# Performance work log

Hardware: AMD Instinct MI355X
Metric: run time of the kernel (lower is better)

## Reference

```python
import jax, jax.numpy as jnp
import numpy as np

B, S, E, D, L, H = 8, 1024, 512, 1024, 8, 16
HD = D // H                 # 64
ROT = max(HD // 2, 32)      # 32
FF = 4 * D
FUSED = 3 * D + 2 * FF      # q,k,v,ff,ff_gate
EPS = 1e-5


def layer_norm(x, w, b):
    mu = jnp.mean(x, axis=-1, keepdims=True)
    var = jnp.mean(jnp.square(x - mu), axis=-1, keepdims=True)
    return (x - mu) * jax.lax.rsqrt(var + EPS) * w + b


def gelu(x):  # fused_gelu from source (erf form, constant 1.41421)
    return x * 0.5 * (1.0 + jax.scipy.special.erf(x / 1.41421))


def silu(x):
    return x * jax.nn.sigmoid(x)


def rotate_half(x):
    x1, x2 = jnp.split(x, 2, axis=-1)
    return jnp.concatenate([-x2, x1], axis=-1)


def rope_tables(seq_len):
    inv = 1.0 / (10000.0 ** (jnp.arange(0, ROT, 2, dtype=jnp.float32) / ROT))
    freqs = jnp.arange(seq_len, dtype=jnp.float32)[:, None] * inv[None, :]
    emb = jnp.concatenate([freqs, freqs], axis=-1)  # [S, ROT]
    # source caches sin/cos in bfloat16 (precision=torch.bfloat16)
    sin = jnp.sin(emb).astype(jnp.bfloat16).astype(jnp.float32)[None, None]
    cos = jnp.cos(emb).astype(jnp.bfloat16).astype(jnp.float32)[None, None]
    return sin, cos  # [1,1,S,ROT]


def setup_inputs() -> dict:
    key = jax.random.key(0)
    ks = jax.random.split(key, 24)
    std = 0.02
    inp = {
        "noisy_embeds": jax.random.normal(ks[0], (B, S, E), jnp.float32),
        "cond_embeds": jax.random.normal(ks[1], (B, S, E), jnp.float32),
        "prev_embeds": jax.random.normal(ks[2], (B, S, E), jnp.float32),
        "infill_mask": jax.random.uniform(ks[3], (B, S, 1), jnp.float32),
        "attention_mask": jnp.zeros((B, 1, 1, S), jnp.float32),
        "times": jax.random.uniform(ks[4], (B,), jnp.float32),
        # time embedding params
        "fourier_w": jax.random.normal(ks[5], (D // 2, 1), jnp.float32),
        "t1_w": jax.random.normal(ks[6], (D, D), jnp.float32) * std,
        "t1_b": jnp.zeros((D,), jnp.float32),
        "t2_w": jax.random.normal(ks[7], (D, D), jnp.float32) * std,
        "t2_b": jnp.zeros((D,), jnp.float32),
        # input projection
        "in_w": jax.random.normal(ks[8], (D, 4 * E), jnp.float32) * std,
        "in_b": jnp.zeros((D,), jnp.float32),
        # per-layer (stacked) block params
        "ln_w": jnp.ones((L, D), jnp.float32),
        "ln_b": jnp.zeros((L, D), jnp.float32),
        "cond_w": jax.random.normal(ks[9], (L, 2 * D, D), jnp.float32) * std,
        "cond_b": jnp.zeros((L, 2 * D), jnp.float32),
        "proj_w": jax.random.normal(ks[10], (L, FUSED, D), jnp.float32) * std,
        "attn_w": jax.random.normal(ks[11], (L, D, D), jnp.float32) * std,
        "attn_b": jnp.zeros((L, D), jnp.float32),
        "ff_w": jax.random.normal(ks[12], (L, D, FF), jnp.float32) * std,
        "ff_b": jnp.zeros((L, D), jnp.float32),
        # output head
        "outln_w": jnp.ones((D,), jnp.float32),
        "outln_b": jnp.zeros((D,), jnp.float32),
        "out_w": jax.random.normal(ks[13], (E, D), jnp.float32) * std,
        "out_b": jnp.zeros((E,), jnp.float32),
        "fin_w": jnp.ones((E,), jnp.float32),
        "fin_b": jnp.zeros((E,), jnp.float32),
    }
    return inp


def _split_heads(x):  # [B,S,H*hd] -> [B,H,S,hd]
    return x.reshape(B, S, H, HD).transpose(0, 2, 1, 3)


def _forward(noisy_embeds, cond_embeds, prev_embeds, infill_mask, attention_mask,
             times, fourier_w, t1_w, t1_b, t2_w, t2_b, in_w, in_b,
             ln_w, ln_b, cond_w, cond_b, proj_w, attn_w, attn_b, ff_w, ff_b,
             outln_w, outln_b, out_w, out_b, fin_w, fin_b):
    # -- time embedding (Random Fourier + MLP) --
    f = 2.0 * np.pi * (times[:, None] @ fourier_w.T)          # [B, D/2]
    te = jnp.concatenate([jnp.cos(f), jnp.sin(f)], axis=-1)   # [B, D]
    te = gelu(te @ t1_w.T + t1_b) @ t2_w.T + t2_b             # [B, D]
    time_embeds = te[:, None, :]                              # [B, 1, D]

    # -- input projection: cat(noisy, cond, prev, mask broadcast) --
    mask_feat = infill_mask * jnp.ones_like(noisy_embeds)     # [B,S,E]
    x = jnp.concatenate([noisy_embeds, cond_embeds, prev_embeds, mask_feat], axis=-1)
    h = x @ in_w.T + in_b                                     # [B,S,D]

    sin, cos = rope_tables(S)
    sm_scale = HD ** (-0.5)

    for i in range(L):
        units = layer_norm(h, ln_w[i], ln_b[i])
        # FiLM conditioning
        sb = silu(time_embeds) @ cond_w[i].T + cond_b[i]      # [B,1,2D]
        scale, bias = jnp.split(sb, 2, axis=-1)
        units = (1.0 + scale) * units + bias
        # fused projection and split
        proj = units @ proj_w[i].T                            # [B,S,11D]
        q, k, v, ff, ff_gate = jnp.split(
            proj, np.cumsum([D, D, D, FF])[:4].tolist(), axis=-1)
        q, k, v = _split_heads(q), _split_heads(k), _split_heads(v)  # [B,H,S,hd]
        # rotary on first ROT dims
        q = jnp.concatenate(
            [q[..., :ROT] * cos + rotate_half(q[..., :ROT]) * sin, q[..., ROT:]], axis=-1)
        k = jnp.concatenate(
            [k[..., :ROT] * cos + rotate_half(k[..., :ROT]) * sin, k[..., ROT:]], axis=-1)
        # NOTE: source scales BOTH q and k by hd^-0.5 (effective hd^-1)
        score = jnp.einsum('bhsd,bhSd->bhsS', q * sm_scale, k * sm_scale)
        score = score + attention_mask
        w = jax.nn.softmax(score, axis=-1)
        attn = jnp.einsum('bhsS,bhSd->bhsd', w, v)
        merged = attn.transpose(0, 2, 1, 3).reshape(B, S, D)
        attn_out = merged @ attn_w[i].T + attn_b[i]
        ff_out = (ff * gelu(ff_gate)) @ ff_w[i].T + ff_b[i]
        h = h + attn_out + ff_out

    out = layer_norm(h, outln_w, outln_b) @ out_w.T + out_b   # [B,S,E]
    return layer_norm(out, fin_w, fin_b)


def reference(noisy_embeds, cond_embeds, prev_embeds, infill_mask, attention_mask,
              times, fourier_w, t1_w, t1_b, t2_w, t2_b, in_w, in_b,
              ln_w, ln_b, cond_w, cond_b, proj_w, attn_w, attn_b, ff_w, ff_b,
              outln_w, outln_b, out_w, out_b, fin_w, fin_b):
    return _forward(noisy_embeds, cond_embeds, prev_embeds, infill_mask, attention_mask,
                    times, fourier_w, t1_w, t1_b, t2_w, t2_b, in_w, in_b,
                    ln_w, ln_b, cond_w, cond_b, proj_w, attn_w, attn_b, ff_w, ff_b,
                    outln_w, outln_b, out_w, out_b, fin_w, fin_b)
```

## Files before the change

### kernel.cpp

```cpp
#include <hip/hip_runtime.h>
#include <hip/hip_bf16.h>
#include <cstddef>
#include <cstdint>

#define BB 8
#define SS 1024
#define EE 512
#define DD 1024
#define LL 8
#define HH 16
#define HD 64
#define ROT 32
#define FF 4096
#define FUSED 11264
#define NTOK 8192

using u16 = unsigned short;
typedef __attribute__((ext_vector_type(8))) __bf16 bf16x8;
typedef __attribute__((ext_vector_type(4))) float f32x4;
typedef __attribute__((ext_vector_type(4))) unsigned short u16x4;
typedef __attribute__((ext_vector_type(8))) unsigned short u16x8;

typedef const __attribute__((address_space(1))) void gas_t;
typedef __attribute__((address_space(3))) void las_t;

__device__ __forceinline__ void gld16(const void* g, void* l) {
  __builtin_amdgcn_global_load_lds((gas_t*)g, (las_t*)l, 16, 0, 0);
}

__device__ __forceinline__ float bf2f(u16 u) {
  union { unsigned int i; float f; } v; v.i = ((unsigned int)u) << 16; return v.f;
}
__device__ __forceinline__ u16 f2bf(float f) {
  union { float f; unsigned int i; } v; v.f = f;
  unsigned int u = v.i;
  unsigned int r = u + 0x7FFFu + ((u >> 16) & 1u);
  return (u16)(r >> 16);
}
__device__ __forceinline__ float gelu_f(float x) {
  return x * 0.5f * (1.0f + erff(x / 1.41421f));
}
__device__ __forceinline__ float silu_f(float x) {
  return x / (1.0f + __expf(-x));
}

template <int ACCUM, int OUTBF16>
__global__ __launch_bounds__(256, 2) void gemm_bt(
    const u16* __restrict__ A, const u16* __restrict__ W,
    const float* __restrict__ bias, void* __restrict__ Cp,
    int M, int N, int K) {
  __shared__ __align__(16) u16 As[128 * 64];
  __shared__ __align__(16) u16 Bs[128 * 64];
  const int tid = threadIdx.x;
  const int w = tid >> 6, lane = tid & 63;
  const int m0 = blockIdx.y * 128, n0 = blockIdx.x * 128;
  const int wm = w >> 1, wn = w & 1;

  f32x4 acc[4][4] = {};

  for (int k0 = 0; k0 < K; k0 += 64) {
#pragma unroll
    for (int i = 0; i < 4; i++) {
      const int c = w + i * 4;
      const int r = c * 8 + (lane >> 3);
      const int colb = ((lane & 7) << 4) ^ ((r & 7) << 4);
      const u16* ga = A + (size_t)(m0 + r) * K + k0 + (colb >> 1);
      gld16(ga, &As[c * 512]);
      const u16* gb = W + (size_t)(n0 + r) * K + k0 + (colb >> 1);
      gld16(gb, &Bs[c * 512]);
    }
    __syncthreads();
#pragma unroll
    for (int ks = 0; ks < 2; ks++) {
      bf16x8 av[4], bv[4];
#pragma unroll
      for (int m = 0; m < 4; m++) {
        const int row = wm * 64 + m * 16 + (lane & 15);
        const int cb = (ks * 64 + ((lane >> 4) << 4)) ^ ((row & 7) << 4);
        av[m] = *(const bf16x8*)((const char*)As + row * 128 + cb);
      }
#pragma unroll
      for (int n = 0; n < 4; n++) {
        const int row = wn * 64 + n * 16 + (lane & 15);
        const int cb = (ks * 64 + ((lane >> 4) << 4)) ^ ((row & 7) << 4);
        bv[n] = *(const bf16x8*)((const char*)Bs + row * 128 + cb);
      }
#pragma unroll
      for (int m = 0; m < 4; m++)
#pragma unroll
        for (int n = 0; n < 4; n++)
          acc[m][n] = __builtin_amdgcn_mfma_f32_16x16x32_bf16(av[m], bv[n], acc[m][n], 0, 0, 0);
    }
    __syncthreads();
  }

  const int colb0 = n0 + wn * 64 + (lane & 15);
  const int rowb0 = m0 + wm * 64 + ((lane >> 4) << 2);
#pragma unroll
  for (int n = 0; n < 4; n++) {
    const int col = colb0 + n * 16;
    const float bn = bias ? bias[col] : 0.0f;
#pragma unroll
    for (int m = 0; m < 4; m++) {
#pragma unroll
      for (int r = 0; r < 4; r++) {
        const size_t idx = (size_t)(rowb0 + m * 16 + r) * N + col;
        const float v = acc[m][n][r] + bn;
        if (ACCUM) {
          ((float*)Cp)[idx] += v;
        } else if (OUTBF16) {
          ((u16*)Cp)[idx] = f2bf(v);
        } else {
          ((float*)Cp)[idx] = v;
        }
      }
    }
  }
}

__global__ __launch_bounds__(256, 2) void attn_fwd(
    const u16* __restrict__ qr, const u16* __restrict__ kr,
    const u16* __restrict__ vt, const float* __restrict__ mask,
    u16* __restrict__ merged) {
  __shared__ __align__(16) u16 Ks[2][128 * 64];
  __shared__ __align__(16) u16 Vs[2][64 * 128];
  __shared__ __align__(16) u16 Ps[4][16 * 128];
  const int tid = threadIdx.x, w = tid >> 6, lane = tid & 63;
  const int g = blockIdx.x;
  const int j = g >> 3;
  const int bh = (g & 7) + ((j >> 4) << 3);
  const int qx = j & 15;
  const int b = bh >> 4;
  const int q0 = qx * 64 + w * 16;
  const u16* Qb = qr + (size_t)bh * SS * HD;
  const u16* Kb = kr + (size_t)bh * SS * HD;
  const u16* Vb = vt + (size_t)bh * HD * SS;
  const float* mb = mask + (size_t)b * SS;

  bf16x8 qf0, qf1;
  {
    const int qrow = q0 + (lane & 15);
    const u16* qp = Qb + (size_t)qrow * HD + ((lane >> 4) << 3);
    qf0 = *(const bf16x8*)qp;
    qf1 = *(const bf16x8*)(qp + 32);
  }

  float mrun[4], srun[4];
  f32x4 acc[4] = {};
#pragma unroll
  for (int r = 0; r < 4; r++) { mrun[r] = -1e30f; srun[r] = 0.0f; }

  u16* pw = &Ps[w][0];

  auto stage = [&](int buf, int kv0) {
#pragma unroll
    for (int i = 0; i < 4; i++) {
      const int c = w + i * 4;
      {
        const int r = c * 8 + (lane >> 3);
        const int colb = ((lane & 7) << 4) ^ ((r & 7) << 4);
        gld16(Kb + (size_t)(kv0 + r) * HD + (colb >> 1), &Ks[buf][c * 512]);
      }
      {
        const int d = c * 4 + (lane >> 4);
        const int colb = ((lane & 15) << 4) ^ ((d & 7) << 4);
        gld16(Vb + (size_t)d * SS + kv0 + (colb >> 1), &Vs[buf][c * 512]);
      }
    }
  };

  stage(0, 0);
  __syncthreads();

  for (int t = 0; t < 8; t++) {
    const int cur = t & 1;
    const int kv0 = t * 128;
    if (t < 7) stage(cur ^ 1, kv0 + 128);

    f32x4 p[8];
    __builtin_amdgcn_s_setprio(1);
#pragma unroll
    for (int blk = 0; blk < 8; blk++) {
      const int row = blk * 16 + (lane & 15);
      const int swz = (row & 7) << 4;
      const bf16x8 k0v = *(const bf16x8*)((const char*)Ks[cur] + row * 128 + ((((lane >> 4) << 4)) ^ swz));
      const bf16x8 k1v = *(const bf16x8*)((const char*)Ks[cur] + row * 128 + ((64 + ((lane >> 4) << 4)) ^ swz));
      f32x4 z = {};
      p[blk] = __builtin_amdgcn_mfma_f32_16x16x32_bf16(qf0, k0v, z, 0, 0, 0);
      p[blk] = __builtin_amdgcn_mfma_f32_16x16x32_bf16(qf1, k1v, p[blk], 0, 0, 0);
    }
    __builtin_amdgcn_s_setprio(0);

    float mv[8];
#pragma unroll
    for (int blk = 0; blk < 8; blk++) mv[blk] = mb[kv0 + blk * 16 + (lane & 15)];
#pragma unroll
    for (int blk = 0; blk < 8; blk++)
#pragma unroll
      for (int r = 0; r < 4; r++) p[blk][r] = p[blk][r] * (1.0f / 64.0f) + mv[blk];

    float fac[4];
#pragma unroll
    for (int r = 0; r < 4; r++) {
      float tm = p[0][r];
#pragma unroll
      for (int blk = 1; blk < 8; blk++) tm = fmaxf(tm, p[blk][r]);
      tm = fmaxf(tm, __shfl_xor(tm, 1));
      tm = fmaxf(tm, __shfl_xor(tm, 2));
      tm = fmaxf(tm, __shfl_xor(tm, 4));
      tm = fmaxf(tm, __shfl_xor(tm, 8));
      const float mn = fmaxf(mrun[r], tm);
      fac[r] = __expf(mrun[r] - mn);
      mrun[r] = mn;
      float rs = 0.0f;
#pragma unroll
      for (int blk = 0; blk < 8; blk++) {
        const float e = __expf(p[blk][r] - mn);
        p[blk][r] = e;
        rs += e;
      }
      rs += __shfl_xor(rs, 1);
      rs += __shfl_xor(rs, 2);
      rs += __shfl_xor(rs, 4);
      rs += __shfl_xor(rs, 8);
      srun[r] = srun[r] * fac[r] + rs;
    }
#pragma unroll
    for (int dblk = 0; dblk < 4; dblk++)
#pragma unroll
      for (int r = 0; r < 4; r++) acc[dblk][r] *= fac[r];

#pragma unroll
    for (int blk = 0; blk < 8; blk++)
#pragma unroll
      for (int r = 0; r < 4; r++) {
        const int q = ((lane >> 4) << 2) + r;
        pw[(q * 128 + blk * 16 + (lane & 15)) ^ ((q & 7) << 3)] = f2bf(p[blk][r]);
      }

    bf16x8 pa[4];
#pragma unroll
    for (int ks = 0; ks < 4; ks++) {
      const int q = lane & 15;
      pa[ks] = *(const bf16x8*)(pw + ((q * 128 + ks * 32 + ((lane >> 4) << 3)) ^ ((q & 7) << 3)));
    }

    __builtin_amdgcn_s_setprio(1);
#pragma unroll
    for (int dblk = 0; dblk < 4; dblk++) {
      const int drow = dblk * 16 + (lane & 15);
      const int swz = (drow & 7) << 4;
#pragma unroll
      for (int ks = 0; ks < 4; ks++) {
        const bf16x8 vv = *(const bf16x8*)((const char*)Vs[cur] + drow * 256 + ((ks * 64 + ((lane >> 4) << 4)) ^ swz));
        acc[dblk] = __builtin_amdgcn_mfma_f32_16x16x32_bf16(pa[ks], vv, acc[dblk], 0, 0, 0);
      }
    }
    __builtin_amdgcn_s_setprio(0);

    __syncthreads();
  }

#pragma unroll
  for (int dblk = 0; dblk < 4; dblk++)
#pragma unroll
    for (int r = 0; r < 4; r++) {
      const int sq = q0 + ((lane >> 4) << 2) + r;
      const int d = dblk * 16 + (lane & 15);
      merged[((size_t)b * SS + sq) * DD + (bh & 15) * HD + d] = f2bf(acc[dblk][r] / srun[r]);
    }
}

__global__ __launch_bounds__(256) void ln_mod(
    const float* __restrict__ x, const float* __restrict__ lw,
    const float* __restrict__ lb, const float* __restrict__ sb,
    u16* __restrict__ out) {
  const int row = blockIdx.x, tid = threadIdx.x;
  const float4 v = ((const float4*)(x + (size_t)row * DD))[tid];
  float vv[4] = {v.x, v.y, v.z, v.w};
  float s = vv[0] + vv[1] + vv[2] + vv[3];
  float q = vv[0] * vv[0] + vv[1] * vv[1] + vv[2] * vv[2] + vv[3] * vv[3];
  for (int off = 1; off < 64; off <<= 1) {
    s += __shfl_xor(s, off);
    q += __shfl_xor(q, off);
  }
  __shared__ float red[8];
  const int w = tid >> 6, lane = tid & 63;
  if (lane == 0) { red[w] = s; red[4 + w] = q; }
  __syncthreads();
  s = red[0] + red[1] + red[2] + red[3];
  q = red[4] + red[5] + red[6] + red[7];
  const float mu = s * (1.0f / DD);
  const float inv = rsqrtf(q * (1.0f / DD) - mu * mu + 1e-5f);
  const int b = row >> 10;
  u16x4 o;
#pragma unroll
  for (int j = 0; j < 4; j++) {
    const int d = tid * 4 + j;
    float g = (vv[j] - mu) * inv * lw[d] + lb[d];
    if (sb) g = (1.0f + sb[(size_t)b * 2048 + d]) * g + sb[(size_t)b * 2048 + DD + d];
    o[j] = f2bf(g);
  }
  *(u16x4*)(out + (size_t)row * DD + tid * 4) = o;
}

__global__ __launch_bounds__(128) void ln_fin(
    const float* __restrict__ x, const float* __restrict__ w_,
    const float* __restrict__ b_, float* __restrict__ out) {
  const int row = blockIdx.x, tid = threadIdx.x;
  const float4 v = ((const float4*)(x + (size_t)row * EE))[tid];
  float vv[4] = {v.x, v.y, v.z, v.w};
  float s = vv[0] + vv[1] + vv[2] + vv[3];
  float q = vv[0] * vv[0] + vv[1] * vv[1] + vv[2] * vv[2] + vv[3] * vv[3];
  for (int off = 1; off < 64; off <<= 1) {
    s += __shfl_xor(s, off);
    q += __shfl_xor(q, off);
  }
  __shared__ float red[4];
  const int w = tid >> 6, lane = tid & 63;
  if (lane == 0) { red[w] = s; red[2 + w] = q; }
  __syncthreads();
  s = red[0] + red[1];
  q = red[2] + red[3];
  const float mu = s * (1.0f / EE);
  const float inv = rsqrtf(q * (1.0f / EE) - mu * mu + 1e-5f);
  float4 o;
  o.x = (vv[0] - mu) * inv * w_[tid * 4 + 0] + b_[tid * 4 + 0];
  o.y = (vv[1] - mu) * inv * w_[tid * 4 + 1] + b_[tid * 4 + 1];
  o.z = (vv[2] - mu) * inv * w_[tid * 4 + 2] + b_[tid * 4 + 2];
  o.w = (vv[3] - mu) * inv * w_[tid * 4 + 3] + b_[tid * 4 + 3];
  ((float4*)(out + (size_t)row * EE))[tid] = o;
}

template <int IA, int OA>
__global__ __launch_bounds__(256) void vec_gemm(
    const float* __restrict__ in, const float* __restrict__ W,
    const float* __restrict__ bias, float* __restrict__ out, int N, int K) {
  const int n = blockIdx.x * 256 + threadIdx.x;
  const int b = blockIdx.y, l = blockIdx.z;
  const float* ir = in + (size_t)b * K;
  const float* wr = W + ((size_t)l * N + n) * K;
  float s = bias[(size_t)l * N + n];
  for (int k = 0; k < K; k += 4) {
    float4 a = *(const float4*)(ir + k);
    const float4 ww = *(const float4*)(wr + k);
    if (IA) { a.x = silu_f(a.x); a.y = silu_f(a.y); a.z = silu_f(a.z); a.w = silu_f(a.w); }
    s += a.x * ww.x + a.y * ww.y + a.z * ww.z + a.w * ww.w;
  }
  if (OA) s = gelu_f(s);
  out[((size_t)l * gridDim.y + b) * N + n] = s;
}

__global__ void time_fourier(const float* __restrict__ times,
                             const float* __restrict__ fw, float* __restrict__ te0) {
  const int j = blockIdx.x * 256 + threadIdx.x;
  const int b = blockIdx.y;
  const float f = 6.28318530717958647692f * times[b] * fw[j];
  te0[(size_t)b * DD + j] = cosf(f);
  te0[(size_t)b * DD + 512 + j] = sinf(f);
}

__global__ void rope_tab(float* __restrict__ st, float* __restrict__ ct) {
  const int s = blockIdx.x;
  const int j = threadIdx.x;
  const int i = j & 15;
  const float inv = powf(10000.0f, -(float)i * (1.0f / 16.0f));
  const float f = (float)s * inv;
  st[s * 32 + j] = bf2f(f2bf(sinf(f)));
  ct[s * 32 + j] = bf2f(f2bf(cosf(f)));
}

__global__ void build_x(const float* __restrict__ a, const float* __restrict__ b,
                        const float* __restrict__ c, const float* __restrict__ m,
                        u16* __restrict__ x) {
  const size_t i4 = ((size_t)blockIdx.x * 256 + threadIdx.x) * 4;
  if (i4 >= (size_t)NTOK * 2048) return;
  const size_t tok = i4 >> 11;
  const int e = (int)(i4 & 2047);
  float4 v;
  if (e < 512)       v = *(const float4*)(a + tok * 512 + e);
  else if (e < 1024) v = *(const float4*)(b + tok * 512 + (e - 512));
  else if (e < 1536) v = *(const float4*)(c + tok * 512 + (e - 1024));
  else { const float mm = m[tok]; v = make_float4(mm, mm, mm, mm); }
  u16x4 o;
  o[0] = f2bf(v.x); o[1] = f2bf(v.y); o[2] = f2bf(v.z); o[3] = f2bf(v.w);
  *(u16x4*)(x + i4) = o;
}

__global__ void rope_qk(const u16* __restrict__ proj, const float* __restrict__ st,
                        const float* __restrict__ ct, u16* __restrict__ q,
                        u16* __restrict__ k) {
  const size_t idx = (size_t)blockIdx.x * 256 + threadIdx.x;
  const size_t tok = idx >> 10;
  const int hd = (int)(idx & 1023);
  const int hh = hd >> 6, d = hd & 63;
  const int s = (int)(tok & 1023);
  const size_t bb = tok >> 10;
  const u16* pr = proj + tok * FUSED;
  float qv = bf2f(pr[hd]);
  float kv = bf2f(pr[DD + hd]);
  if (d < ROT) {
    const float cs = ct[s * 32 + d], sn = st[s * 32 + d];
    const int pidx = hd - d + ((d < 16) ? d + 16 : d - 16);
    const float qp = bf2f(pr[pidx]);
    const float kp = bf2f(pr[DD + pidx]);
    const float sg = (d < 16) ? -1.0f : 1.0f;
    qv = qv * cs + sg * qp * sn;
    kv = kv * cs + sg * kp * sn;
  }
  const size_t o = ((bb * HH + hh) * SS + s) * HD + d;
  q[o] = f2bf(qv);
  k[o] = f2bf(kv);
}

__global__ __launch_bounds__(256) void transp_v(const u16* __restrict__ proj,
                                                u16* __restrict__ v) {
  __shared__ u16 tile[64 * 72];
  const int tid = threadIdx.x;
  const int s0 = blockIdx.x * 64, h = blockIdx.y, b = blockIdx.z;
  {
    const int sl = tid >> 2, qd = (tid & 3) * 16;
    const u16* src = proj + (size_t)(b * SS + s0 + sl) * FUSED + 2 * DD + h * 64 + qd;
    const u16x8 a0 = *(const u16x8*)src;
    const u16x8 a1 = *(const u16x8*)(src + 8);
    *(u16x8*)&tile[sl * 72 + qd] = a0;
    *(u16x8*)&tile[sl * 72 + qd + 8] = a1;
  }
  __syncthreads();
  {
    const int dl = tid >> 2, qs = (tid & 3) * 16;
    u16x8 o0, o1;
#pragma unroll
    for (int j = 0; j < 8; j++) o0[j] = tile[(qs + j) * 72 + dl];
#pragma unroll
    for (int j = 0; j < 8; j++) o1[j] = tile[(qs + 8 + j) * 72 + dl];
    u16* dst = v + ((size_t)(b * HH + h) * HD + dl) * SS + s0 + qs;
    *(u16x8*)dst = o0;
    *(u16x8*)(dst + 8) = o1;
  }
}

__global__ void gate_k(const u16* __restrict__ proj, u16* __restrict__ ff) {
  const size_t i8 = ((size_t)blockIdx.x * 256 + threadIdx.x) * 8;
  const size_t tok = i8 >> 12;
  const int f = (int)(i8 & 4095);
  const u16* pr = proj + tok * FUSED + 3 * DD + f;
  const u16x8 a = *(const u16x8*)pr;
  const u16x8 g = *(const u16x8*)(pr + FF);
  u16x8 o;
#pragma unroll
  for (int j = 0; j < 8; j++) o[j] = f2bf(bf2f(a[j]) * gelu_f(bf2f(g[j])));
  *(u16x8*)(ff + i8) = o;
}

__global__ void cast_bf16(const float* __restrict__ in, u16* __restrict__ out, size_t n4) {
  const size_t i = (size_t)blockIdx.x * 256 + threadIdx.x;
  if (i >= n4) return;
  const float4 v = ((const float4*)in)[i];
  u16x4 o;
  o[0] = f2bf(v.x); o[1] = f2bf(v.y); o[2] = f2bf(v.z); o[3] = f2bf(v.w);
  ((u16x4*)out)[i] = o;
}

extern "C" void kernel_launch(void* const* d_in, const int* in_sizes, int n_in,
                              void* d_out, int out_size, void* d_ws, size_t ws_size,
                              hipStream_t stream) {
  const float* noisy   = (const float*)d_in[0];
  const float* condi   = (const float*)d_in[1];
  const float* prev    = (const float*)d_in[2];
  const float* infill  = (const float*)d_in[3];
  const float* amask   = (const float*)d_in[4];
  const float* times   = (const float*)d_in[5];
  const float* fourier = (const float*)d_in[6];
  const float* t1_w    = (const float*)d_in[7];
  const float* t1_b    = (const float*)d_in[8];
  const float* t2_w    = (const float*)d_in[9];
  const float* t2_b    = (const float*)d_in[10];
  const float* in_w    = (const float*)d_in[11];
  const float* in_b    = (const float*)d_in[12];
  const float* ln_w    = (const float*)d_in[13];
  const float* ln_b    = (const float*)d_in[14];
  const float* cond_w  = (const float*)d_in[15];
  const float* cond_b  = (const float*)d_in[16];
  const float* proj_w  = (const float*)d_in[17];
  const float* attn_w  = (const float*)d_in[18];
  const float* attn_b  = (const float*)d_in[19];
  const float* ff_w    = (const float*)d_in[20];
  const float* ff_b    = (const float*)d_in[21];
  const float* outln_w = (const float*)d_in[22];
  const float* outln_b = (const float*)d_in[23];
  const float* out_w   = (const float*)d_in[24];
  const float* out_b   = (const float*)d_in[25];
  const float* fin_w   = (const float*)d_in[26];
  const float* fin_b   = (const float*)d_in[27];
  float* outp = (float*)d_out;

  char* p = (char*)d_ws;
  auto alloc = [&](size_t bytes) -> char* {
    char* r = p;
    p += (bytes + 255) & ~(size_t)255;
    return r;
  };
  u16* in_w_h   = (u16*)alloc((size_t)DD * 2048 * 2);
  u16* proj_w_h = (u16*)alloc((size_t)LL * FUSED * DD * 2);
  u16* attn_w_h = (u16*)alloc((size_t)LL * DD * DD * 2);
  u16* ff_w_h   = (u16*)alloc((size_t)LL * DD * FF * 2);
  u16* out_w_h  = (u16*)alloc((size_t)EE * DD * 2);
  float* te0 = (float*)alloc((size_t)BB * DD * 4);
  float* te1 = (float*)alloc((size_t)BB * DD * 4);
  float* te2 = (float*)alloc((size_t)BB * DD * 4);
  float* sb  = (float*)alloc((size_t)LL * BB * 2048 * 4);
  float* stab = (float*)alloc((size_t)SS * 32 * 4);
  float* ctab = (float*)alloc((size_t)SS * 32 * 4);
  u16* xb    = (u16*)alloc((size_t)NTOK * 2048 * 2);
  float* h   = (float*)alloc((size_t)NTOK * DD * 4);
  u16* units = (u16*)alloc((size_t)NTOK * DD * 2);
  u16* projb = (u16*)alloc((size_t)NTOK * FUSED * 2);
  u16* qrb   = (u16*)alloc((size_t)NTOK * DD * 2);
  u16* krb   = (u16*)alloc((size_t)NTOK * DD * 2);
  u16* vtb   = (u16*)alloc((size_t)NTOK * DD * 2);
  u16* mg    = (u16*)alloc((size_t)NTOK * DD * 2);
  u16* ffa   = (u16*)alloc((size_t)NTOK * FF * 2);
  u16* hn    = (u16*)alloc((size_t)NTOK * DD * 2);
  float* ob  = (float*)alloc((size_t)NTOK * EE * 4);

  auto castN = [&](const float* src, u16* dst, size_t n) {
    const size_t n4 = n / 4;
    cast_bf16<<<dim3((unsigned)((n4 + 255) / 256)), dim3(256), 0, stream>>>(src, dst, n4);
  };
  castN(in_w, in_w_h, (size_t)DD * 2048);
  castN(proj_w, proj_w_h, (size_t)LL * FUSED * DD);
  castN(attn_w, attn_w_h, (size_t)LL * DD * DD);
  castN(ff_w, ff_w_h, (size_t)LL * DD * FF);
  castN(out_w, out_w_h, (size_t)EE * DD);

  time_fourier<<<dim3(2, BB), 256, 0, stream>>>(times, fourier, te0);
  vec_gemm<0, 1><<<dim3(4, BB, 1), 256, 0, stream>>>(te0, t1_w, t1_b, te1, 1024, 1024);
  vec_gemm<0, 0><<<dim3(4, BB, 1), 256, 0, stream>>>(te1, t2_w, t2_b, te2, 1024, 1024);
  vec_gemm<1, 0><<<dim3(8, BB, LL), 256, 0, stream>>>(te2, cond_w, cond_b, sb, 2048, 1024);
  rope_tab<<<SS, 32, 0, stream>>>(stab, ctab);
  build_x<<<16384, 256, 0, stream>>>(noisy, condi, prev, infill, xb);
  gemm_bt<0, 0><<<dim3(DD / 128, NTOK / 128), 256, 0, stream>>>(xb, in_w_h, in_b, h, NTOK, DD, 2048);

  for (int l = 0; l < LL; l++) {
    ln_mod<<<NTOK, 256, 0, stream>>>(h, ln_w + (size_t)l * DD, ln_b + (size_t)l * DD,
                                     sb + (size_t)l * BB * 2048, units);
    gemm_bt<0, 1><<<dim3(FUSED / 128, NTOK / 128), 256, 0, stream>>>(
        units, proj_w_h + (size_t)l * FUSED * DD, nullptr, projb, NTOK, FUSED, DD);
    rope_qk<<<32768, 256, 0, stream>>>(projb, stab, ctab, qrb, krb);
    transp_v<<<dim3(SS / 64, HH, BB), 256, 0, stream>>>(projb, vtb);
    gate_k<<<16384, 256, 0, stream>>>(projb, ffa);
    attn_fwd<<<dim3(2048), 256, 0, stream>>>(qrb, krb, vtb, amask, mg);
    gemm_bt<1, 0><<<dim3(DD / 128, NTOK / 128), 256, 0, stream>>>(
        mg, attn_w_h + (size_t)l * DD * DD, attn_b + (size_t)l * DD, h, NTOK, DD, DD);
    gemm_bt<1, 0><<<dim3(DD / 128, NTOK / 128), 256, 0, stream>>>(
        ffa, ff_w_h + (size_t)l * DD * FF, ff_b + (size_t)l * DD, h, NTOK, DD, FF);
  }

  ln_mod<<<NTOK, 256, 0, stream>>>(h, outln_w, outln_b, nullptr, hn);
  gemm_bt<0, 0><<<dim3(EE / 128, NTOK / 128), 256, 0, stream>>>(hn, out_w_h, out_b, ob, NTOK, EE, DD);
  ln_fin<<<NTOK, 128, 0, stream>>>(ob, fin_w, fin_b, outp);
}
```

Before: 5.216 ms.

## Fuse GELU gating into FF projection GEMM and double-buffer GEMM LDS

Splits the fused projection into a QKV GEMM and a separate FF/gate GEMM whose weights are reordered so that each ff row and its matching gate row land in adjacent 16-column tiles. The gating (ff * gelu(gate)) then runs in the GEMM epilogue, which drops the gate_k kernel and the write and re-read of the 8192-wide bf16 intermediate. The GEMM also gains double-buffered LDS staging (prefetching the next K tile while computing) and s_setprio around the MFMA loop. Doubling LDS per block may lower occupancy, and the gated GEMM keeps fp32 accumulators for the gating rather than rounding them to bf16 first.

```diff
diff --git a/kernel.cpp b/kernel.cpp
--- a/kernel.cpp
+++ b/kernel.cpp
@@ -14,6 +14,7 @@
 #define FF 4096
 #define FUSED 11264
 #define NTOK 8192
+#define QKVW 3072
 
 using u16 = unsigned short;
 typedef __attribute__((ext_vector_type(8))) __bf16 bf16x8;
@@ -44,13 +45,13 @@
   return x / (1.0f + __expf(-x));
 }
 
-template <int ACCUM, int OUTBF16>
+template <int ACCUM, int OUTBF16, int GATED>
 __global__ __launch_bounds__(256, 2) void gemm_bt(
     const u16* __restrict__ A, const u16* __restrict__ W,
     const float* __restrict__ bias, void* __restrict__ Cp,
     int M, int N, int K) {
-  __shared__ __align__(16) u16 As[128 * 64];
-  __shared__ __align__(16) u16 Bs[128 * 64];
+  __shared__ __align__(16) u16 As[2][128 * 64];
+  __shared__ __align__(16) u16 Bs[2][128 * 64];
   const int tid = threadIdx.x;
   const int w = tid >> 6, lane = tid & 63;
   const int m0 = blockIdx.y * 128, n0 = blockIdx.x * 128;
@@ -58,18 +59,25 @@
 
   f32x4 acc[4][4] = {};
 
-  for (int k0 = 0; k0 < K; k0 += 64) {
+  auto stage = [&](int buf, int k0) {
 #pragma unroll
     for (int i = 0; i < 4; i++) {
       const int c = w + i * 4;
       const int r = c * 8 + (lane >> 3);
       const int colb = ((lane & 7) << 4) ^ ((r & 7) << 4);
-      const u16* ga = A + (size_t)(m0 + r) * K + k0 + (colb >> 1);
-      gld16(ga, &As[c * 512]);
-      const u16* gb = W + (size_t)(n0 + r) * K + k0 + (colb >> 1);
-      gld16(gb, &Bs[c * 512]);
-    }
-    __syncthreads();
+      gld16(A + (size_t)(m0 + r) * K + k0 + (colb >> 1), &As[buf][c * 512]);
+      gld16(W + (size_t)(n0 + r) * K + k0 + (colb >> 1), &Bs[buf][c * 512]);
+    }
+  };
+
+  stage(0, 0);
+  __syncthreads();
+
+  for (int k0 = 0; k0 < K; k0 += 64) {
+    const int cur = (k0 >> 6) & 1;
+    if (k0 + 64 < K) stage(cur ^ 1, k0 + 64);
+
+    __builtin_amdgcn_s_setprio(1);
 #pragma unroll
     for (int ks = 0; ks < 2; ks++) {
       bf16x8 av[4], bv[4];
@@ -77,13 +85,13 @@
       for (int m = 0; m < 4; m++) {
         const int row = wm * 64 + m * 16 + (lane & 15);
         const int cb = (ks * 64 + ((lane >> 4) << 4)) ^ ((row & 7) << 4);
-        av[m] = *(const bf16x8*)((const char*)As + row * 128 + cb);
+        av[m] = *(const bf16x8*)((const char*)As[cur] + row * 128 + cb);
       }
 #pragma unroll
       for (int n = 0; n < 4; n++) {
         const int row = wn * 64 + n * 16 + (lane & 15);
         const int cb = (ks * 64 + ((lane >> 4) << 4)) ^ ((row & 7) << 4);
-        bv[n] = *(const bf16x8*)((const char*)Bs + row * 128 + cb);
+        bv[n] = *(const bf16x8*)((const char*)Bs[cur] + row * 128 + cb);
       }
 #pragma unroll
       for (int m = 0; m < 4; m++)
@@ -91,11 +99,28 @@
         for (int n = 0; n < 4; n++)
           acc[m][n] = __builtin_amdgcn_mfma_f32_16x16x32_bf16(av[m], bv[n], acc[m][n], 0, 0, 0);
     }
+    __builtin_amdgcn_s_setprio(0);
     __syncthreads();
   }
 
+  const int rowb0 = m0 + wm * 64 + ((lane >> 4) << 2);
+  if (GATED) {
+    const int No = N >> 1;
+#pragma unroll
+    for (int n = 0; n < 4; n += 2) {
+      const int outcol = (n0 >> 1) + wn * 32 + ((n >> 1) << 4) + (lane & 15);
+#pragma unroll
+      for (int m = 0; m < 4; m++)
+#pragma unroll
+        for (int r = 0; r < 4; r++) {
+          const float fv = acc[m][n][r];
+          const float gv = acc[m][n + 1][r];
+          ((u16*)Cp)[(size_t)(rowb0 + m * 16 + r) * No + outcol] = f2bf(fv * gelu_f(gv));
+        }
+    }
+    return;
+  }
   const int colb0 = n0 + wn * 64 + (lane & 15);
-  const int rowb0 = m0 + wm * 64 + ((lane >> 4) << 2);
 #pragma unroll
   for (int n = 0; n < 4; n++) {
     const int col = colb0 + n * 16;
@@ -396,7 +421,7 @@
   const int hh = hd >> 6, d = hd & 63;
   const int s = (int)(tok & 1023);
   const size_t bb = tok >> 10;
-  const u16* pr = proj + tok * FUSED;
+  const u16* pr = proj + tok * QKVW;
   float qv = bf2f(pr[hd]);
   float kv = bf2f(pr[DD + hd]);
   if (d < ROT) {
@@ -420,7 +445,7 @@
   const int s0 = blockIdx.x * 64, h = blockIdx.y, b = blockIdx.z;
   {
     const int sl = tid >> 2, qd = (tid & 3) * 16;
-    const u16* src = proj + (size_t)(b * SS + s0 + sl) * FUSED + 2 * DD + h * 64 + qd;
+    const u16* src = proj + (size_t)(b * SS + s0 + sl) * QKVW + 2 * DD + h * 64 + qd;
     const u16x8 a0 = *(const u16x8*)src;
     const u16x8 a1 = *(const u16x8*)(src + 8);
     *(u16x8*)&tile[sl * 72 + qd] = a0;
@@ -438,19 +463,6 @@
     *(u16x8*)dst = o0;
     *(u16x8*)(dst + 8) = o1;
   }
-}
-
-__global__ void gate_k(const u16* __restrict__ proj, u16* __restrict__ ff) {
-  const size_t i8 = ((size_t)blockIdx.x * 256 + threadIdx.x) * 8;
-  const size_t tok = i8 >> 12;
-  const int f = (int)(i8 & 4095);
-  const u16* pr = proj + tok * FUSED + 3 * DD + f;
-  const u16x8 a = *(const u16x8*)pr;
-  const u16x8 g = *(const u16x8*)(pr + FF);
-  u16x8 o;
-#pragma unroll
-  for (int j = 0; j < 8; j++) o[j] = f2bf(bf2f(a[j]) * gelu_f(bf2f(g[j])));
-  *(u16x8*)(ff + i8) = o;
 }
 
 __global__ void cast_bf16(const float* __restrict__ in, u16* __restrict__ out, size_t n4) {
@@ -460,6 +472,35 @@
   u16x4 o;
   o[0] = f2bf(v.x); o[1] = f2bf(v.y); o[2] = f2bf(v.z); o[3] = f2bf(v.w);
   ((u16x4*)out)[i] = o;
+}
+
+__global__ void cast_q(const float* __restrict__ src, u16* __restrict__ dst) {
+  const int i = blockIdx.x * 256 + threadIdx.x;
+  const int l = blockIdx.y;
+  const int r = i >> 7, cb = (i & 127) * 8;
+  const float* s = src + ((size_t)l * FUSED + r) * DD + cb;
+  const float4 a = *(const float4*)s;
+  const float4 b = *(const float4*)(s + 4);
+  u16x8 o;
+  o[0] = f2bf(a.x); o[1] = f2bf(a.y); o[2] = f2bf(a.z); o[3] = f2bf(a.w);
+  o[4] = f2bf(b.x); o[5] = f2bf(b.y); o[6] = f2bf(b.z); o[7] = f2bf(b.w);
+  *(u16x8*)(dst + ((size_t)l * QKVW + r) * DD + cb) = o;
+}
+
+__global__ void cast_ffg(const float* __restrict__ src, u16* __restrict__ dst) {
+  const int i = blockIdx.x * 256 + threadIdx.x;
+  const int l = blockIdx.y;
+  const int r = i >> 7, cb = (i & 127) * 8;
+  const int t16 = r >> 4, pos = r & 15;
+  const int j = (t16 >> 1) * 16 + pos;
+  const int srow = (t16 & 1) ? (3 * DD + FF + j) : (3 * DD + j);
+  const float* s = src + ((size_t)l * FUSED + srow) * DD + cb;
+  const float4 a = *(const float4*)s;
+  const float4 b = *(const float4*)(s + 4);
+  u16x8 o;
+  o[0] = f2bf(a.x); o[1] = f2bf(a.y); o[2] = f2bf(a.z); o[3] = f2bf(a.w);
+  o[4] = f2bf(b.x); o[5] = f2bf(b.y); o[6] = f2bf(b.z); o[7] = f2bf(b.w);
+  *(u16x8*)(dst + ((size_t)l * 8192 + r) * DD + cb) = o;
 }
 
 extern "C" void kernel_launch(void* const* d_in, const int* in_sizes, int n_in,
@@ -502,7 +543,8 @@
     return r;
   };
   u16* in_w_h   = (u16*)alloc((size_t)DD * 2048 * 2);
-  u16* proj_w_h = (u16*)alloc((size_t)LL * FUSED * DD * 2);
+  u16* projq_w_h = (u16*)alloc((size_t)LL * QKVW * DD * 2);
+  u16* ffg_w_h  = (u16*)alloc((size_t)LL * 8192 * DD * 2);
   u16* attn_w_h = (u16*)alloc((size_t)LL * DD * DD * 2);
   u16* ff_w_h   = (u16*)alloc((size_t)LL * DD * FF * 2);
   u16* out_w_h  = (u16*)alloc((size_t)EE * DD * 2);
@@ -515,7 +557,7 @@
   u16* xb    = (u16*)alloc((size_t)NTOK * 2048 * 2);
   float* h   = (float*)alloc((size_t)NTOK * DD * 4);
   u16* units = (u16*)alloc((size_t)NTOK * DD * 2);
-  u16* projb = (u16*)alloc((size_t)NTOK * FUSED * 2);
+  u16* projq = (u16*)alloc((size_t)NTOK * QKVW * 2);
   u16* qrb   = (u16*)alloc((size_t)NTOK * DD * 2);
   u16* krb   = (u16*)alloc((size_t)NTOK * DD * 2);
   u16* vtb   = (u16*)alloc((size_t)NTOK * DD * 2);
@@ -529,7 +571,8 @@
     cast_bf16<<<dim3((unsigned)((n4 + 255) / 256)), dim3(256), 0, stream>>>(src, dst, n4);
   };
   castN(in_w, in_w_h, (size_t)DD * 2048);
-  castN(proj_w, proj_w_h, (size_t)LL * FUSED * DD);
+  cast_q<<<dim3(QKVW * 128 / 256, LL), 256, 0, stream>>>(proj_w, projq_w_h);
+  cast_ffg<<<dim3(8192 * 128 / 256, LL), 256, 0, stream>>>(proj_w, ffg_w_h);
   castN(attn_w, attn_w_h, (size_t)LL * DD * DD);
   castN(ff_w, ff_w_h, (size_t)LL * DD * FF);
   castN(out_w, out_w_h, (size_t)EE * DD);
@@ -540,24 +583,25 @@
   vec_gemm<1, 0><<<dim3(8, BB, LL), 256, 0, stream>>>(te2, cond_w, cond_b, sb, 2048, 1024);
   rope_tab<<<SS, 32, 0, stream>>>(stab, ctab);
   build_x<<<16384, 256, 0, stream>>>(noisy, condi, prev, infill, xb);
-  gemm_bt<0, 0><<<dim3(DD / 128, NTOK / 128), 256, 0, stream>>>(xb, in_w_h, in_b, h, NTOK, DD, 2048);
+  gemm_bt<0, 0, 0><<<dim3(DD / 128, NTOK / 128), 256, 0, stream>>>(xb, in_w_h, in_b, h, NTOK, DD, 2048);
 
   for (int l = 0; l < LL; l++) {
     ln_mod<<<NTOK, 256, 0, stream>>>(h, ln_w + (size_t)l * DD, ln_b + (size_t)l * DD,
                                      sb + (size_t)l * BB * 2048, units);
-    gemm_bt<0, 1><<<dim3(FUSED / 128, NTOK / 128), 256, 0, stream>>>(
-        units, proj_w_h + (size_t)l * FUSED * DD, nullptr, projb, NTOK, FUSED, DD);
-    rope_qk<<<32768, 256, 0, stream>>>(projb, stab, ctab, qrb, krb);
-    transp_v<<<dim3(SS / 64, HH, BB), 256, 0, stream>>>(projb, vtb);
-    gate_k<<<16384, 256, 0, stream>>>(projb, ffa);
+    gemm_bt<0, 1, 0><<<dim3(QKVW / 128, NTOK / 128), 256, 0, stream>>>(
+        units, projq_w_h + (size_t)l * QKVW * DD, nullptr, projq, NTOK, QKVW, DD);
+    gemm_bt<0, 0, 1><<<dim3(8192 / 128, NTOK / 128), 256, 0, stream>>>(
+        units, ffg_w_h + (size_t)l * 8192 * DD, nullptr, ffa, NTOK, 8192, DD);
+    rope_qk<<<32768, 256, 0, stream>>>(projq, stab, ctab, qrb, krb);
+    transp_v<<<dim3(SS / 64, HH, BB), 256, 0, stream>>>(projq, vtb);
     attn_fwd<<<dim3(2048), 256, 0, stream>>>(qrb, krb, vtb, amask, mg);
-    gemm_bt<1, 0><<<dim3(DD / 128, NTOK / 128), 256, 0, stream>>>(
+    gemm_bt<1, 0, 0><<<dim3(DD / 128, NTOK / 128), 256, 0, stream>>>(
         mg, attn_w_h + (size_t)l * DD * DD, attn_b + (size_t)l * DD, h, NTOK, DD, DD);
-    gemm_bt<1, 0><<<dim3(DD / 128, NTOK / 128), 256, 0, stream>>>(
+    gemm_bt<1, 0, 0><<<dim3(DD / 128, NTOK / 128), 256, 0, stream>>>(
         ffa, ff_w_h + (size_t)l * DD * FF, ff_b + (size_t)l * DD, h, NTOK, DD, FF);
   }
 
   ln_mod<<<NTOK, 256, 0, stream>>>(h, outln_w, outln_b, nullptr, hn);
-  gemm_bt<0, 0><<<dim3(EE / 128, NTOK / 128), 256, 0, stream>>>(hn, out_w_h, out_b, ob, NTOK, EE, DD);
+  gemm_bt<0, 0, 0><<<dim3(EE / 128, NTOK / 128), 256, 0, stream>>>(hn, out_w_h, out_b, ob, NTOK, EE, DD);
   ln_fin<<<NTOK, 128, 0, stream>>>(ob, fin_w, fin_b, outp);
 }
```

Result: no change. 5.125 ms (-1.8%).
